# Kernel optimization log

Measured on AMD Instinct MI355X. Metric: run time of the kernel, lower is better.

## Reference

```python
import jax, jax.numpy as jnp
import numpy as np

N = 2900000
B = 4096
D = 768
GAMMA = 0.8
EPS = 1e-14
TAU_MIN, TAU_MAX = 0.005, 0.05
RHO = 8.0
ETA_INIT = 0.03
BETA_U = 0.5
GRAD_CLIP = 5.0
TAU_INIT = 0.01


def setup_inputs() -> dict:
    key = jax.random.key(0)
    k1, k2, k3, k4, k5, k6 = jax.random.split(key, 6)
    img = jax.random.normal(k1, (B, D), jnp.float32)
    img = img / jnp.linalg.norm(img, axis=-1, keepdims=True)  # CLIP-style unit-norm embeddings
    txt = jax.random.normal(k2, (B, D), jnp.float32)
    txt = txt / jnp.linalg.norm(txt, axis=-1, keepdims=True)
    image_ids = jax.random.randint(k3, (B,), 0, N, dtype=jnp.int32)
    text_ids = jax.random.randint(k4, (B,), 0, N, dtype=jnp.int32)
    return {
        "image_features": img,
        "text_features": txt,
        "image_ids": image_ids,
        "text_ids": text_ids,
        "epoch": 1,
        "max_epoch": 30,
        "s_I": jax.random.uniform(k5, (N,), jnp.float32),
        "s_T": jax.random.uniform(k6, (N,), jnp.float32),
        "b_I": jnp.zeros((N,), jnp.float32),
        "b_T": jnp.zeros((N,), jnp.float32),
        "u_I": jnp.zeros((N,), jnp.float32),
        "u_T": jnp.zeros((N,), jnp.float32),
        "tau_I": jnp.full((N,), TAU_INIT, jnp.float32),
        "tau_T": jnp.full((N,), TAU_INIT, jnp.float32),
    }


def reference(image_features, text_features, image_ids, text_ids, epoch, max_epoch,
              s_I, s_T, b_I, b_T, u_I, u_T, tau_I, tau_T):
    sim = jnp.einsum("id,jd->ij", image_features, text_features)  # [B, B]
    diag_sim = jnp.diagonal(sim)
    bsz = sim.shape[0]
    mask_neg = 1.0 - jnp.eye(bsz, dtype=sim.dtype)

    tau_image = tau_I[image_ids]  # [B]
    tau_text = tau_T[text_ids]    # [B]

    image_diffs = sim - diag_sim[:, None]
    text_diffs = sim - diag_sim[None, :]
    # torch .detach() -> stop_gradient; everything downstream of these is detached too
    idt = jax.lax.stop_gradient(image_diffs / tau_image[:, None])
    tdt = jax.lax.stop_gradient(text_diffs / tau_text[None, :])

    old_b_I = b_I[image_ids]
    new_b_I = jnp.maximum(jnp.max(idt, axis=1), old_b_I)  # running row-max
    old_b_T = b_T[text_ids]
    new_b_T = jnp.maximum(jnp.max(tdt, axis=0), old_b_T)  # running col-max

    exp_i = jnp.exp(idt - new_b_I[:, None]) * mask_neg
    exp_t = jnp.exp(tdt - new_b_T[None, :]) * mask_neg
    g_I = jnp.sum(exp_i, axis=1)  # [B]
    g_T = jnp.sum(exp_t, axis=0)  # [B]

    if epoch == 0:
        sI = g_I
        sT = g_T
    else:
        sI = (1.0 - GAMMA) * s_I[image_ids] * jnp.exp(old_b_I - new_b_I) + GAMMA * g_I
        sT = (1.0 - GAMMA) * s_T[text_ids] * jnp.exp(old_b_T - new_b_T) + GAMMA * g_T

    sI_c = jnp.maximum(sI, EPS)
    sT_c = jnp.maximum(sT, EPS)

    w_i = exp_i / sI_c[:, None]
    w_t = exp_t / sT_c[None, :]

    image_loss = jnp.sum(w_i * image_diffs, axis=1)  # [B]
    text_loss = jnp.sum(w_t * text_diffs, axis=0)    # [B]
    total_loss = image_loss.mean() + text_loss.mean()

    twi = jnp.log(sI_c / (bsz - 1)) + new_b_I + RHO - jnp.sum(w_i * idt, axis=1)
    twt = jnp.log(sT_c / (bsz - 1)) + new_b_T + RHO - jnp.sum(w_t * tdt, axis=0)

    u_I_b = (1.0 - BETA_U) * u_I[image_ids] + BETA_U * jnp.clip(twi, -GRAD_CLIP, GRAD_CLIP)
    u_T_b = (1.0 - BETA_U) * u_T[text_ids] + BETA_U * jnp.clip(twt, -GRAD_CLIP, GRAD_CLIP)
    tau_I_b = jnp.clip(tau_image - ETA_INIT * u_I_b, TAU_MIN, TAU_MAX)
    tau_T_b = jnp.clip(tau_text - ETA_INIT * u_T_b, TAU_MIN, TAU_MAX)

    # torch mutates the persistent buffers in place; expose the updates as outputs
    b_I_new = b_I.at[image_ids].set(new_b_I)
    b_T_new = b_T.at[text_ids].set(new_b_T)
    s_I_new = s_I.at[image_ids].set(sI)
    s_T_new = s_T.at[text_ids].set(sT)
    u_I_new = u_I.at[image_ids].set(u_I_b)
    u_T_new = u_T.at[text_ids].set(u_T_b)
    tau_I_new = tau_I.at[image_ids].set(tau_I_b)
    tau_T_new = tau_T.at[text_ids].set(tau_T_b)

    return (total_loss, tau_image, tau_text,
            s_I_new, s_T_new, b_I_new, b_T_new, u_I_new, u_T_new, tau_I_new, tau_T_new)
```

## Files before the change

kernel.cpp:

```cpp
#include <hip/hip_runtime.h>
#include <hip/hip_bf16.h>
#include <math.h>

#define N_ITEMS 2900000
#define BDIM 4096
#define DDIM 768

typedef float f32x4 __attribute__((ext_vector_type(4)));
typedef __bf16 bf16x8 __attribute__((ext_vector_type(8)));

__device__ inline unsigned short f2bf(float f) {
    unsigned int u = __float_as_uint(f);
    unsigned int lsb = (u >> 16) & 1u;
    u += 0x7fffu + lsb;
    return (unsigned short)(u >> 16);
}

__device__ inline void gload16(const void* g, void* l) {
    __builtin_amdgcn_global_load_lds(
        (const __attribute__((address_space(1))) void*)g,
        (__attribute__((address_space(3))) void*)l, 16, 0, 0);
}

__global__ __launch_bounds__(256) void prep_kernel(
        const float* __restrict__ img, const float* __restrict__ txt,
        const int* __restrict__ image_ids, const int* __restrict__ text_ids,
        const float* __restrict__ tau_I, const float* __restrict__ tau_T,
        unsigned short* __restrict__ Xbf, unsigned short* __restrict__ Ybf,
        float* __restrict__ diag, float* __restrict__ tau_row,
        float* __restrict__ out) {
    const int bx = blockIdx.x;
    if (bx < 1536) {
        const int per = (BDIM * DDIM) / 4;
        for (int u = bx * 256 + threadIdx.x; u < 2 * per; u += 1536 * 256) {
            const float4* src = (u < per) ? (const float4*)img : (const float4*)txt;
            unsigned short* dst = (u < per) ? Xbf : Ybf;
            int i = (u < per) ? u : u - per;
            float4 v = src[i];
            ushort4 o;
            o.x = f2bf(v.x); o.y = f2bf(v.y); o.z = f2bf(v.z); o.w = f2bf(v.w);
            ((ushort4*)dst)[i] = o;
        }
        return;
    }
    const int w = (bx - 1536) * 4 + (threadIdx.x >> 6);
    const int lane = threadIdx.x & 63;
    const float* a = img + (size_t)w * DDIM;
    const float* b = txt + (size_t)w * DDIM;
    float s = 0.f;
    for (int d = lane; d < DDIM; d += 64) s += a[d] * b[d];
    #pragma unroll
    for (int d = 32; d >= 1; d >>= 1) s += __shfl_xor(s, d);
    if (lane == 0) diag[w] = s;
    if (lane == 1) {
        float t = tau_I[image_ids[w]];
        tau_row[w] = t;
        out[1 + w] = t;
    }
    if (lane == 2) {
        float t = tau_T[text_ids[w]];
        tau_row[BDIM + w] = t;
        out[1 + BDIM + w] = t;
    }
}

__global__ __launch_bounds__(512) void gemm_kernel(
        const unsigned short* __restrict__ Xbf, const unsigned short* __restrict__ Ybf,
        const float* __restrict__ diag, const float* __restrict__ tau_row,
        float* __restrict__ partials ,
        const float* s0, const float* s1, const float* s2, const float* s3,
        const float* s4, const float* s5, const float* s6, const float* s7,
        float* __restrict__ cdst ) {
    __shared__ unsigned short As[2][16384];
    __shared__ unsigned short Bs[2][16384];

    const int cb = blockIdx.x, rb = blockIdx.y;
    const int t = threadIdx.x;
    const int wave = t >> 6, lane = t & 63;
    const int wr = wave >> 2, wc = wave & 3;
    const int g = lane >> 4, r16 = lane & 15;

    f32x4 acc[8][4];
    #pragma unroll
    for (int m = 0; m < 8; m++)
        #pragma unroll
        for (int n = 0; n < 4; n++)
            #pragma unroll
            for (int q = 0; q < 4; q++) acc[m][n][q] = 0.f;

    const int srow = t >> 3;
    const int sgr  = (t & 7) ^ (srow & 7);
    const unsigned short* pA[4];
    const unsigned short* pB[4];
    #pragma unroll
    for (int i = 0; i < 4; i++) {
        pA[i] = Xbf + (size_t)(rb * 256 + i * 64 + srow) * DDIM + sgr * 8;
        pB[i] = Ybf + (size_t)(cb * 256 + i * 64 + srow) * DDIM + sgr * 8;
    }

    #define STAGE(buf, kk) do {                                                   \
        const size_t ko_ = (size_t)(kk) * 64;                                     \
        _Pragma("unroll")                                                         \
        for (int i_ = 0; i_ < 4; i_++) {                                          \
            gload16(pA[i_] + ko_, (char*)As + (buf)*32768 + i_*8192 + wave*1024); \
            gload16(pB[i_] + ko_, (char*)Bs + (buf)*32768 + i_*8192 + wave*1024); \
        }                                                                         \
    } while (0)

    const int gtid = (rb * 16 + cb) * 512 + t;
    f32x4 cval[4];
    int cu_[4];
    auto srcp = [&](int k) -> const float* {
        switch (k) {
            case 0: return s0; case 1: return s1; case 2: return s2; case 3: return s3;
            case 4: return s4; case 5: return s5; case 6: return s6; default: return s7;
        }
    };
    auto CLOAD = [&](int slot, int c) {
        const int u = c * 131072 + gtid;
        cu_[slot] = u;
        if (u < 5800000) {
            const int k = u / 725000;
            const int i = u - k * 725000;
            cval[slot] = __builtin_nontemporal_load((const f32x4*)srcp(k) + i);
        }
    };
    auto CSTORE = [&](int slot) {
        const int u = cu_[slot];
        if (u < 5800000) {
            const int k = u / 725000;
            const int i = u - k * 725000;
            float* dd = cdst + (size_t)k * N_ITEMS + (size_t)i * 4;
            __builtin_nontemporal_store(cval[slot][0], dd + 0);
            __builtin_nontemporal_store(cval[slot][1], dd + 1);
            __builtin_nontemporal_store(cval[slot][2], dd + 2);
            __builtin_nontemporal_store(cval[slot][3], dd + 3);
        }
    };

    STAGE(0, 0);
    #pragma unroll
    for (int j = 0; j < 4; j++) CLOAD(j, j);
    __syncthreads();

    int cur = 0;
    for (int kk = 0; kk < 12; ++kk) {
        if (kk < 11) STAGE(cur ^ 1, kk + 1);
        #pragma unroll
        for (int j = 0; j < 4; j++) {
            CSTORE(j);
            if (kk < 11) CLOAD(j, (kk + 1) * 4 + j);
        }
        const char* Ac = (const char*)As + cur * 32768;
        const char* Bc = (const char*)Bs + cur * 32768;
        #pragma unroll
        for (int ks = 0; ks < 2; ++ks) {
            bf16x8 af[8], bfr[4];
            #pragma unroll
            for (int m = 0; m < 8; m++) {
                const int row = wr * 128 + m * 16 + r16;
                const int gr = (ks * 4 + g) ^ (r16 & 7);
                af[m] = *(const bf16x8*)(Ac + row * 128 + gr * 16);
            }
            #pragma unroll
            for (int n = 0; n < 4; n++) {
                const int row = wc * 64 + n * 16 + r16;
                const int gr = (ks * 4 + g) ^ (r16 & 7);
                bfr[n] = *(const bf16x8*)(Bc + row * 128 + gr * 16);
            }
            #pragma unroll
            for (int m = 0; m < 8; m++)
                #pragma unroll
                for (int n = 0; n < 4; n++)
                    acc[m][n] = __builtin_amdgcn_mfma_f32_16x16x32_bf16(af[m], bfr[n], acc[m][n], 0, 0, 0);
        }
        __syncthreads();
        cur ^= 1;
    }
    #undef STAGE

    const int R0 = rb * 256 + wr * 128;
    const int C0 = cb * 256 + wc * 64;

    #pragma unroll
    for (int m = 0; m < 8; m++) {
        #pragma unroll
        for (int q = 0; q < 4; q++) {
            const int rowg = R0 + m * 16 + g * 4 + q;
            const float dgv = diag[rowg];
            const float itau = 1.0f / tau_row[rowg];
            float x4[4];
            float mloc = -3.0e38f;
            #pragma unroll
            for (int n = 0; n < 4; n++) {
                const int colg = C0 + n * 16 + r16;
                const float x = (acc[m][n][q] - dgv) * itau;
                x4[n] = x;
                mloc = (colg != rowg) ? fmaxf(mloc, x) : mloc;
            }
            #pragma unroll
            for (int d = 1; d < 16; d <<= 1) mloc = fmaxf(mloc, __shfl_xor(mloc, d));
            float E = 0.f, F = 0.f;
            #pragma unroll
            for (int n = 0; n < 4; n++) {
                const int colg = C0 + n * 16 + r16;
                const float e = (colg != rowg) ? __expf(x4[n] - mloc) : 0.f;
                E += e; F += e * x4[n];
            }
            #pragma unroll
            for (int d = 1; d < 16; d <<= 1) {
                E += __shfl_xor(E, d);
                F += __shfl_xor(F, d);
            }
            if (r16 == 0) {
                const int chunk = cb * 4 + wc;
                float* pp = partials + (((size_t)rowg) * 64 + chunk) * 3;
                pp[0] = mloc; pp[1] = E; pp[2] = F;
            }
        }
    }

    #pragma unroll
    for (int n = 0; n < 4; n++) {
        const int colg = C0 + n * 16 + r16;
        const float dgc = diag[colg];
        const float itc = 1.0f / tau_row[BDIM + colg];
        float mloc = -3.0e38f;
        #pragma unroll
        for (int m = 0; m < 8; m++)
            #pragma unroll
            for (int q = 0; q < 4; q++) {
                const int rowg = R0 + m * 16 + g * 4 + q;
                const float x = (acc[m][n][q] - dgc) * itc;
                mloc = (rowg != colg) ? fmaxf(mloc, x) : mloc;
            }
        mloc = fmaxf(mloc, __shfl_xor(mloc, 16));
        mloc = fmaxf(mloc, __shfl_xor(mloc, 32));
        float E = 0.f, F = 0.f;
        #pragma unroll
        for (int m = 0; m < 8; m++)
            #pragma unroll
            for (int q = 0; q < 4; q++) {
                const int rowg = R0 + m * 16 + g * 4 + q;
                const float x = (acc[m][n][q] - dgc) * itc;
                const float e = (rowg != colg) ? __expf(x - mloc) : 0.f;
                E += e; F += e * x;
            }
        E += __shfl_xor(E, 16); F += __shfl_xor(F, 16);
        E += __shfl_xor(E, 32); F += __shfl_xor(F, 32);
        if (g == 0) {
            const int rchunk = rb * 2 + wr;
            float* pp = partials + (((size_t)BDIM + colg) * 64 + rchunk) * 3;
            pp[0] = mloc; pp[1] = E; pp[2] = F;
        }
    }
}

__global__ __launch_bounds__(256) void tail_kernel(
        const float* __restrict__ partials,
        const int* __restrict__ image_ids, const int* __restrict__ text_ids,
        const float* __restrict__ b_I, const float* __restrict__ b_T,
        const float* __restrict__ s_I, const float* __restrict__ s_T,
        const float* __restrict__ u_I, const float* __restrict__ u_T,
        const float* __restrict__ tau_row, const int* __restrict__ epoch_ptr,
        float* __restrict__ loss_arr, float* __restrict__ out) {
    __shared__ int sids[BDIM];
    const int bx = blockIdx.x;
    const int p = bx >> 10;
    const int* ids = p ? text_ids : image_ids;
    for (int i = threadIdx.x; i < BDIM / 4; i += 256)
        ((int4*)sids)[i] = ((const int4*)ids)[i];

    const int wave = threadIdx.x >> 6, lane = threadIdx.x & 63;
    const int row = (bx & 1023) * 4 + wave;
    float m, E, F;
    if (p == 1 && lane >= 32) {
        m = -3.0e38f; E = 0.f; F = 0.f;
    } else {
        const float* pp = partials + (((size_t)p * BDIM + row) * 64 + lane) * 3;
        m = pp[0]; E = pp[1]; F = pp[2];
    }
    #pragma unroll
    for (int d = 1; d < 64; d <<= 1) {
        float mo = __shfl_xor(m, d), Eo = __shfl_xor(E, d), Fo = __shfl_xor(F, d);
        float mn = fmaxf(m, mo);
        float a1 = expf(m - mn), a2 = expf(mo - mn);
        E = E * a1 + Eo * a2;
        F = F * a1 + Fo * a2;
        m = mn;
    }
    const int id = ids[row];
    const float ob = p ? b_T[id] : b_I[id];
    const float so = p ? s_T[id] : s_I[id];
    const float uo = p ? u_T[id] : u_I[id];
    const float tv = tau_row[p * BDIM + row];
    const float m0 = fmaxf(ob, 0.0f);
    if (m0 > m) { float sc = expf(m - m0); E *= sc; F *= sc; m = m0; }
    float sI = (*epoch_ptr == 0) ? E : 0.2f * so * expf(ob - m) + 0.8f * E;
    float sc_ = fmaxf(sI, 1e-14f);
    float ratio = F / sc_;
    float twi = logf(sc_ * (1.0f / 4095.0f)) + m + 8.0f - ratio;
    float uc = fminf(fmaxf(twi, -5.0f), 5.0f);
    float ub = 0.5f * uo + 0.5f * uc;
    float tb = fminf(fmaxf(tv - 0.03f * ub, 0.005f), 0.05f);
    if (lane == 0) loss_arr[p * BDIM + row] = tv * ratio;

    __syncthreads();
    const int myid = sids[row];
    bool dup = false;
    for (int c = row + 1 + lane; c < BDIM; c += 64)
        dup |= (sids[c] == myid);
    if (__any(dup)) return;
    if (lane < 4) {
        const float v = (lane == 0) ? m : (lane == 1) ? sI : (lane == 2) ? ub : tb;
        const int arr = (lane == 0) ? (2 + p) : (lane == 1) ? (0 + p)
                      : (lane == 2) ? (4 + p) : (6 + p);
        out[8193 + (size_t)arr * N_ITEMS + myid] = v;
    }
}

__global__ void loss_kernel(const float* __restrict__ loss_arr, float* __restrict__ out) {
    __shared__ float wsum[16];
    int t = threadIdx.x;
    float s = 0.f;
    for (int i = t; i < 2 * BDIM; i += 1024) s += loss_arr[i];
    #pragma unroll
    for (int d = 32; d >= 1; d >>= 1) s += __shfl_xor(s, d);
    if ((t & 63) == 0) wsum[t >> 6] = s;
    __syncthreads();
    if (t == 0) {
        float tot = 0.f;
        for (int i = 0; i < 16; i++) tot += wsum[i];
        out[0] = tot * (1.0f / (float)BDIM);
    }
}

extern "C" void kernel_launch(void* const* d_in, const int* in_sizes, int n_in,
                              void* d_out, int out_size, void* d_ws, size_t ws_size,
                              hipStream_t stream) {
    const float* img       = (const float*)d_in[0];
    const float* txt       = (const float*)d_in[1];
    const int*   image_ids = (const int*)d_in[2];
    const int*   text_ids  = (const int*)d_in[3];
    const int*   epoch     = (const int*)d_in[4];
    const float* s_I   = (const float*)d_in[6];
    const float* s_T   = (const float*)d_in[7];
    const float* b_I   = (const float*)d_in[8];
    const float* b_T   = (const float*)d_in[9];
    const float* u_I   = (const float*)d_in[10];
    const float* u_T   = (const float*)d_in[11];
    const float* tau_I = (const float*)d_in[12];
    const float* tau_T = (const float*)d_in[13];
    float* out = (float*)d_out;

    char* ws = (char*)d_ws;
    unsigned short* Xbf = (unsigned short*)ws;
    unsigned short* Ybf = (unsigned short*)(ws + 6291456);
    float* diag     = (float*)(ws + 12582912);
    float* tau_row  = (float*)(ws + 12599296);
    float* partials = (float*)(ws + 12632064);
    float* loss_arr = (float*)(ws + 18923520);

    prep_kernel<<<2560, 256, 0, stream>>>(img, txt, image_ids, text_ids, tau_I, tau_T,
                                          Xbf, Ybf, diag, tau_row, out);
    gemm_kernel<<<dim3(16, 16), 512, 0, stream>>>(Xbf, Ybf, diag, tau_row, partials,
                                                  s_I, s_T, b_I, b_T, u_I, u_T,
                                                  tau_I, tau_T, out + 8193);
    tail_kernel<<<2048, 256, 0, stream>>>(partials, image_ids, text_ids,
                                          b_I, b_T, s_I, s_T, u_I, u_T,
                                          tau_row, epoch, loss_arr, out);
    loss_kernel<<<1, 1024, 0, stream>>>(loss_arr, out);
}
```

Baseline: 104.4 us.

## Split GEMM k-loop into four barrier-separated phases interleaving loads and MFMAs

Restructures the main bf16 MFMA loop into four phases per k-tile. Each phase issues part of the next tile's global-to-LDS loads and one slot of the state-copy stream, reads half the A fragments, then runs 16 MFMAs at raised wave priority with explicit waitcnt and sched barriers. The aim is to spread memory traffic evenly across compute and to lower register pressure by holding only half the A fragments at a time. In exchange it adds more barriers per tile and depends on manual scheduling hints.

```diff
diff --git a/kernel.cpp b/kernel.cpp
--- a/kernel.cpp
+++ b/kernel.cpp
@@ -98,15 +98,6 @@
         pB[i] = Ybf + (size_t)(cb * 256 + i * 64 + srow) * DDIM + sgr * 8;
     }
 
-    #define STAGE(buf, kk) do {                                                   \
-        const size_t ko_ = (size_t)(kk) * 64;                                     \
-        _Pragma("unroll")                                                         \
-        for (int i_ = 0; i_ < 4; i_++) {                                          \
-            gload16(pA[i_] + ko_, (char*)As + (buf)*32768 + i_*8192 + wave*1024); \
-            gload16(pB[i_] + ko_, (char*)Bs + (buf)*32768 + i_*8192 + wave*1024); \
-        }                                                                         \
-    } while (0)
-
     const int gtid = (rb * 16 + cb) * 512 + t;
     f32x4 cval[4];
     int cu_[4];
@@ -138,46 +129,70 @@
         }
     };
 
-    STAGE(0, 0);
+    #pragma unroll
+    for (int i = 0; i < 4; i++) {
+        gload16(pA[i], (char*)As + i * 8192 + wave * 1024);
+        gload16(pB[i], (char*)Bs + i * 8192 + wave * 1024);
+    }
     #pragma unroll
     for (int j = 0; j < 4; j++) CLOAD(j, j);
-    __syncthreads();
-
-    int cur = 0;
+
+    #define PHASE(ks, h, EXTRA) do {                                              \
+        EXTRA;                                                                    \
+        bf16x8 af[4], bfr[4];                                                     \
+        const int gr_ = ((ks) * 4 + g) ^ (r16 & 7);                               \
+        _Pragma("unroll")                                                         \
+        for (int m_ = 0; m_ < 4; m_++)                                            \
+            af[m_] = *(const bf16x8*)(Ac + (wr*128 + ((h)*4+m_)*16 + r16)*128 + gr_*16); \
+        _Pragma("unroll")                                                         \
+        for (int n_ = 0; n_ < 4; n_++)                                            \
+            bfr[n_] = *(const bf16x8*)(Bc + (wc*64 + n_*16 + r16)*128 + gr_*16);  \
+        asm volatile("s_waitcnt lgkmcnt(0)" ::: "memory");                        \
+        __builtin_amdgcn_sched_barrier(0);                                        \
+        __builtin_amdgcn_s_setprio(1);                                            \
+        _Pragma("unroll")                                                         \
+        for (int m_ = 0; m_ < 4; m_++)                                            \
+            _Pragma("unroll")                                                     \
+            for (int n_ = 0; n_ < 4; n_++)                                        \
+                acc[(h)*4+m_][n_] = __builtin_amdgcn_mfma_f32_16x16x32_bf16(      \
+                    af[m_], bfr[n_], acc[(h)*4+m_][n_], 0, 0, 0);                 \
+        __builtin_amdgcn_s_setprio(0);                                            \
+        __builtin_amdgcn_s_barrier();                                             \
+        __builtin_amdgcn_sched_barrier(0);                                        \
+    } while (0)
+
     for (int kk = 0; kk < 12; ++kk) {
-        if (kk < 11) STAGE(cur ^ 1, kk + 1);
-        #pragma unroll
-        for (int j = 0; j < 4; j++) {
-            CSTORE(j);
-            if (kk < 11) CLOAD(j, (kk + 1) * 4 + j);
-        }
-        const char* Ac = (const char*)As + cur * 32768;
-        const char* Bc = (const char*)Bs + cur * 32768;
-        #pragma unroll
-        for (int ks = 0; ks < 2; ++ks) {
-            bf16x8 af[8], bfr[4];
-            #pragma unroll
-            for (int m = 0; m < 8; m++) {
-                const int row = wr * 128 + m * 16 + r16;
-                const int gr = (ks * 4 + g) ^ (r16 & 7);
-                af[m] = *(const bf16x8*)(Ac + row * 128 + gr * 16);
-            }
-            #pragma unroll
-            for (int n = 0; n < 4; n++) {
-                const int row = wc * 64 + n * 16 + r16;
-                const int gr = (ks * 4 + g) ^ (r16 & 7);
-                bfr[n] = *(const bf16x8*)(Bc + row * 128 + gr * 16);
-            }
-            #pragma unroll
-            for (int m = 0; m < 8; m++)
-                #pragma unroll
-                for (int n = 0; n < 4; n++)
-                    acc[m][n] = __builtin_amdgcn_mfma_f32_16x16x32_bf16(af[m], bfr[n], acc[m][n], 0, 0, 0);
-        }
-        __syncthreads();
-        cur ^= 1;
-    }
-    #undef STAGE
+        const char* Ac = (const char*)As + (kk & 1) * 32768;
+        const char* Bc = (const char*)Bs + (kk & 1) * 32768;
+        char* An = (char*)As + ((kk & 1) ^ 1) * 32768;
+        char* Bn = (char*)Bs + ((kk & 1) ^ 1) * 32768;
+        const size_t ko = (size_t)(kk + 1) * 64;
+        const bool more = (kk < 11);
+        asm volatile("s_waitcnt vmcnt(0)" ::: "memory");
+        __builtin_amdgcn_s_barrier();
+        __builtin_amdgcn_sched_barrier(0);
+        PHASE(0, 0, {
+            if (more) { gload16(pA[0]+ko, An + 0*8192 + wave*1024);
+                        gload16(pA[1]+ko, An + 1*8192 + wave*1024); }
+            CSTORE(0); if (more) CLOAD(0, (kk+1)*4 + 0);
+        });
+        PHASE(0, 1, {
+            if (more) { gload16(pA[2]+ko, An + 2*8192 + wave*1024);
+                        gload16(pA[3]+ko, An + 3*8192 + wave*1024); }
+            CSTORE(1); if (more) CLOAD(1, (kk+1)*4 + 1);
+        });
+        PHASE(1, 0, {
+            if (more) { gload16(pB[0]+ko, Bn + 0*8192 + wave*1024);
+                        gload16(pB[1]+ko, Bn + 1*8192 + wave*1024); }
+            CSTORE(2); if (more) CLOAD(2, (kk+1)*4 + 2);
+        });
+        PHASE(1, 1, {
+            if (more) { gload16(pB[2]+ko, Bn + 2*8192 + wave*1024);
+                        gload16(pB[3]+ko, Bn + 3*8192 + wave*1024); }
+            CSTORE(3); if (more) CLOAD(3, (kk+1)*4 + 3);
+        });
+    }
+    #undef PHASE
 
     const int R0 = rb * 256 + wr * 128;
     const int C0 = cb * 256 + wc * 64;
```

New measurement: 118.0 us. 1.13x slower.
